# Kernel optimization log

Measured on AMD Instinct MI355X. Metric: run time of the kernel, lower is better.

Reference implementation:

```python
import jax, jax.numpy as jnp
import numpy as np

B, T, DIN, DC, CS = 8, 4096, 1024, 256, 8192
EPS = 1e-12

def _l2norm(x):
    # F.normalize: x / max(||x||_2, eps) along last axis
    n = jnp.sqrt(jnp.sum(x * x, axis=-1, keepdims=True))
    return x / jnp.maximum(n, EPS)

def _wn(v, g):
    # torch weight_norm(dim=0): w = g * v / ||v|| per output row
    n = jnp.sqrt(jnp.sum(v * v, axis=1, keepdims=True))
    return g * v / jnp.maximum(n, EPS)

def setup_inputs() -> dict:
    key = jax.random.key(0)
    k = jax.random.split(key, 4)
    return {
        "z": jax.random.normal(k[0], (B, DIN, T), jnp.float32),
        "in_v": jax.random.normal(k[1], (DC, DIN), jnp.float32) * 0.02,
        "in_g": jnp.ones((DC, 1), jnp.float32),
        "in_b": jnp.zeros((DC,), jnp.float32),
        "out_v": jax.random.normal(k[2], (DIN, DC), jnp.float32) * 0.02,
        "out_g": jnp.ones((DIN, 1), jnp.float32),
        "out_b": jnp.zeros((DIN,), jnp.float32),
        "codebook": jax.random.normal(k[3], (CS, DC), jnp.float32),
    }

def reference(z, in_v, in_g, in_b, out_v, out_g, out_b, codebook):
    b, _, t = z.shape
    w_in = _wn(in_v, in_g)                      # (DC, DIN)
    z_e = jnp.einsum('bdt,cd->bct', z, w_in) + in_b[None, :, None]  # (B, DC, T)

    # decode_latents (eval mode: dropout p=0)
    enc = _l2norm(z_e.transpose(0, 2, 1).reshape(b * t, -1))   # (BT, DC)
    cb = _l2norm(codebook)                                     # (CS, DC)
    dist = (jnp.sum(enc * enc, axis=1, keepdims=True)
            - 2.0 * enc @ cb.T
            + jnp.sum(cb * cb, axis=1)[None, :])               # (BT, CS)
    indices = jnp.argmax(-dist, axis=1).reshape(b, t)          # (B, T)
    z_q = codebook[indices].transpose(0, 2, 1)                 # (B, DC, T)

    commitment_loss = jnp.mean((z_e - jax.lax.stop_gradient(z_q)) ** 2, axis=(1, 2))
    codebook_loss = jnp.mean((z_q - jax.lax.stop_gradient(z_e)) ** 2, axis=(1, 2))

    z_q_st = z_e + jax.lax.stop_gradient(z_q - z_e)            # straight-through
    w_out = _wn(out_v, out_g)                                  # (DIN, DC)
    z_q_out = jnp.einsum('bct,dc->bdt', z_q_st, w_out) + out_b[None, :, None]
    return (z_q_out, commitment_loss, codebook_loss, indices)
```

## Files before the change

kernel.cpp:

```cpp
#include <hip/hip_runtime.h>
#include <stdint.h>

#define BB 8
#define TT 4096
#define DIN 1024
#define DC 256
#define CS 8192
#define EPSF 1e-12f

typedef unsigned short ushort_t;
typedef __attribute__((ext_vector_type(8))) short short8;
typedef __attribute__((ext_vector_type(4))) float f32x4;

constexpr size_t OFF_WIN   = 0;
constexpr size_t OFF_WOUTT = OFF_WIN   + 1048576;
constexpr size_t OFF_CBN   = OFF_WOUTT + 1048576;
constexpr size_t OFF_NRM2  = OFF_CBN   + 8388608;
constexpr size_t OFF_ZE    = OFF_NRM2  + 32768;
constexpr size_t OFF_INV   = OFF_ZE    + 33554432;
constexpr size_t OFF_ENC2  = OFF_INV   + 131072;
constexpr size_t OFF_KEYS  = OFF_ENC2  + 131072;
constexpr size_t OFF_LOSS  = OFF_KEYS  + 262144;
constexpr size_t OFF_WSPL  = OFF_LOSS  + 256;
constexpr size_t OFF_W2T   = OFF_WSPL  + 1048576;
constexpr size_t REQ_WS_ZE = OFF_W2T + 134217728ull;

__device__ __forceinline__ float block_reduce_sum_256(float v, float* sbuf) {
  #pragma unroll
  for (int o = 32; o > 0; o >>= 1) v += __shfl_down(v, o, 64);
  int lane = threadIdx.x & 63, w = threadIdx.x >> 6;
  if (lane == 0) sbuf[w] = v;
  __syncthreads();
  float r = sbuf[0] + sbuf[1] + sbuf[2] + sbuf[3];
  __syncthreads();
  return r;
}

__device__ __forceinline__ ushort_t bf16_rne(float x) {
  unsigned u = __float_as_uint(x);
  unsigned r = (u + 0x7FFFu + ((u >> 16) & 1u)) >> 16;
  return (ushort_t)r;
}
__device__ __forceinline__ float bf16f(ushort_t h) {
  return __uint_as_float(((unsigned)h) << 16);
}

__device__ __forceinline__ int swz4(int r) {
  return (r + (r >> 2)) & 3;
}

__device__ __forceinline__ void async_copy16(const ushort_t* g, ushort_t* lds) {
  __builtin_amdgcn_global_load_lds(
      (const __attribute__((address_space(1))) void*)g,
      (__attribute__((address_space(3))) void*)lds, 16, 0, 0);
}

__device__ __forceinline__ void stage_tile8(const ushort_t* __restrict__ s0,
                                            ushort_t* __restrict__ dstbuf,
                                            const int (&go)[8]) {
  #pragma unroll
  for (int i = 0; i < 8; i++) async_copy16(s0 + go[i], dstbuf + i*512);
}

__device__ __forceinline__ void stage2(const ushort_t* __restrict__ srcbase,
                                       ushort_t* __restrict__ comp,
                                       const int (&go)[2], int wu) {
  async_copy16(srcbase + go[0], comp + wu);
  async_copy16(srcbase + go[1], comp + wu + 4096);
}

#define LD8(base, off) (*(const short8*)((const char*)(base) + (off)))

template<int MH, int CLO>
__device__ __forceinline__ void qmfma(f32x4 (&acc)[8][4],
    const short8 (&fah)[4], const short8 (&fal)[4],
    const short8 (&fbh)[4], const short8 (&fbl)[4]) {
  #pragma unroll
  for (int r = 0; r < 4; r++) {
    #pragma unroll
    for (int c2 = 0; c2 < 2; c2++) {
      f32x4 t = acc[MH*4 + r][CLO + c2];
      t = __builtin_amdgcn_mfma_f32_16x16x32_bf16(fah[r], fbh[CLO + c2], t, 0, 0, 0);
      t = __builtin_amdgcn_mfma_f32_16x16x32_bf16(fal[r], fbh[CLO + c2], t, 0, 0, 0);
      t = __builtin_amdgcn_mfma_f32_16x16x32_bf16(fah[r], fbl[CLO + c2], t, 0, 0, 0);
      acc[MH*4 + r][CLO + c2] = t;
    }
  }
}

__global__ void k_prep_win(const float* __restrict__ v, const float* __restrict__ g,
                           float* __restrict__ w, ushort_t* __restrict__ wh,
                           ushort_t* __restrict__ wl) {
  __shared__ float sb[4];
  int r = blockIdx.x, t = threadIdx.x;
  float xv[4]; float s = 0.f;
  #pragma unroll
  for (int i = 0; i < 4; i++) { xv[i] = v[r*DIN + t + i*256]; s += xv[i]*xv[i]; }
  s = block_reduce_sum_256(s, sb);
  float sc = g[r] / fmaxf(sqrtf(s), EPSF);
  #pragma unroll
  for (int i = 0; i < 4; i++) {
    float val = xv[i] * sc;
    int idx = r*DIN + t + i*256;
    w[idx] = val;
    ushort_t h = bf16_rne(val);
    wh[idx] = h;
    wl[idx] = bf16_rne(val - bf16f(h));
  }
}

__global__ void k_prep_wout(const float* __restrict__ v, const float* __restrict__ g,
                            float* __restrict__ wT) {
  __shared__ float sb[4];
  int r = blockIdx.x, t = threadIdx.x;
  float x = v[r*DC + t];
  float s = block_reduce_sum_256(x*x, sb);
  float sc = g[r] / fmaxf(sqrtf(s), EPSF);
  wT[t*DIN + r] = x * sc;
}

__global__ void k_prep_cb(const float* __restrict__ cb, ushort_t* __restrict__ cbh,
                          ushort_t* __restrict__ cbl, float* __restrict__ nrm2,
                          float* __restrict__ nmraw, float* __restrict__ n2raw,
                          ushort_t* __restrict__ crh, ushort_t* __restrict__ crl) {
  __shared__ float sb[4];
  int j = blockIdx.x, t = threadIdx.x;
  float x = cb[j*DC + t];
  ushort_t hr = bf16_rne(x);
  crh[j*DC + t] = hr;
  crl[j*DC + t] = bf16_rne(x - bf16f(hr));
  float s = block_reduce_sum_256(x*x, sb);
  float nm = fmaxf(sqrtf(s), EPSF);
  float cn = x / nm;
  ushort_t h = bf16_rne(cn);
  cbh[j*DC + t] = h;
  cbl[j*DC + t] = bf16_rne(cn - bf16f(h));
  float q = block_reduce_sum_256(cn*cn, sb);
  if (t == 0) { nrm2[j] = q; nmraw[j] = nm; n2raw[j] = s; }
}

__global__ void k_split_wout(const float* __restrict__ v, const float* __restrict__ g,
                             ushort_t* __restrict__ wh, ushort_t* __restrict__ wl) {
  __shared__ float sb[4];
  int r = blockIdx.x, t = threadIdx.x;
  float x = v[r*DC + t];
  float s = block_reduce_sum_256(x*x, sb);
  float sc = g[r] / fmaxf(sqrtf(s), EPSF);
  float val = x * sc;
  ushort_t h = bf16_rne(val);
  wh[r*DC + t] = h;
  wl[r*DC + t] = bf16_rne(val - bf16f(h));
}

template<bool BIAS>
__global__ __launch_bounds__(256) void k_gemm(
    const float* __restrict__ A, const float* __restrict__ Bmat,
    const float* __restrict__ bias, float* __restrict__ C,
    int K, int lda, int ldb, int ldc, size_t strideB, size_t strideC)
{
  __shared__ float As[16][132];
  __shared__ float Bs[16][132];
  const int bn = blockIdx.x * 128;
  const int bm = blockIdx.y * 128;
  const float* Bb = Bmat + (size_t)blockIdx.z * strideB;
  float* Cb = C + (size_t)blockIdx.z * strideC;
  const int tid = threadIdx.x;
  const int tx = tid & 15, ty = tid >> 4;
  const int am = tid & 127, akq = (tid >> 7) * 8;
  const int bk = tid >> 5, bj = (tid & 31) * 4;

  float acc[8][8];
  #pragma unroll
  for (int i = 0; i < 8; i++)
    #pragma unroll
    for (int j = 0; j < 8; j++) acc[i][j] = 0.f;

  for (int k0 = 0; k0 < K; k0 += 16) {
    float4 a0 = *(const float4*)&A[(size_t)(bm+am)*lda + k0 + akq];
    float4 a1 = *(const float4*)&A[(size_t)(bm+am)*lda + k0 + akq + 4];
    float4 b0 = *(const float4*)&Bb[(size_t)(k0+bk)*ldb + bn + bj];
    float4 b1 = *(const float4*)&Bb[(size_t)(k0+bk+8)*ldb + bn + bj];
    As[akq+0][am] = a0.x; As[akq+1][am] = a0.y; As[akq+2][am] = a0.z; As[akq+3][am] = a0.w;
    As[akq+4][am] = a1.x; As[akq+5][am] = a1.y; As[akq+6][am] = a1.z; As[akq+7][am] = a1.w;
    *(float4*)&Bs[bk][bj] = b0;
    *(float4*)&Bs[bk+8][bj] = b1;
    __syncthreads();
    #pragma unroll
    for (int k = 0; k < 16; k++) {
      float av[8], bv[8];
      float4 x0 = *(const float4*)&As[k][tx*4];
      float4 x1 = *(const float4*)&As[k][tx*4+64];
      float4 y0 = *(const float4*)&Bs[k][ty*4];
      float4 y1 = *(const float4*)&Bs[k][ty*4+64];
      av[0]=x0.x; av[1]=x0.y; av[2]=x0.z; av[3]=x0.w;
      av[4]=x1.x; av[5]=x1.y; av[6]=x1.z; av[7]=x1.w;
      bv[0]=y0.x; bv[1]=y0.y; bv[2]=y0.z; bv[3]=y0.w;
      bv[4]=y1.x; bv[5]=y1.y; bv[6]=y1.z; bv[7]=y1.w;
      #pragma unroll
      for (int i = 0; i < 8; i++)
        #pragma unroll
        for (int j = 0; j < 8; j++)
          acc[i][j] += av[i] * bv[j];
    }
    __syncthreads();
  }

  #pragma unroll
  for (int i = 0; i < 8; i++) {
    int mm = bm + ((i < 4) ? tx*4 + i : 64 + tx*4 + (i-4));
    float bia = BIAS ? bias[mm] : 0.f;
    float4 v0 = make_float4(acc[i][0]+bia, acc[i][1]+bia, acc[i][2]+bia, acc[i][3]+bia);
    float4 v1 = make_float4(acc[i][4]+bia, acc[i][5]+bia, acc[i][6]+bia, acc[i][7]+bia);
    *(float4*)&Cb[(size_t)mm*ldc + bn + ty*4]      = v0;
    *(float4*)&Cb[(size_t)mm*ldc + bn + 64 + ty*4] = v1;
  }
}

__global__ __launch_bounds__(512) void k_ze_enc(
    const float* __restrict__ z,
    const ushort_t* __restrict__ wh, const ushort_t* __restrict__ wl,
    const float* __restrict__ in_b,
    ushort_t* __restrict__ ehi, ushort_t* __restrict__ elo,
    float* __restrict__ inv, float* __restrict__ enc2, float* __restrict__ e2raw)
{
  __shared__ ushort_t smem[49152];
  __shared__ float e2s[128][4];
  __shared__ float sIv[128];

  ushort_t* sAh = smem;
  ushort_t* sAl = smem + 8192;
  ushort_t* sBh = smem + 16384;
  ushort_t* sBl = smem + 32768;

  const int t0 = blockIdx.x * 128;
  const int b  = blockIdx.y;
  const int tid = threadIdx.x;
  const int lane = tid & 63;
  const int wave = tid >> 6;
  const int wr = wave >> 2, wc = wave & 3;
  const int ml = lane & 15, quad = lane >> 4;
  const size_t r0 = (size_t)b*TT + t0;

  const int dl = tid >> 4, tg = tid & 15;
  const float* zsrc = z + (size_t)b*DIN*TT + (size_t)dl*TT + t0 + tg*8;
  int idxA[8];
  #pragma unroll
  for (int i = 0; i < 8; i++) {
    int t = tg*8 + i;
    idxA[i] = t*32 + (((dl >> 3) ^ swz4(t)) << 3) + (dl & 7);
  }

  int goB[2];
  #pragma unroll
  for (int l = 0; l < 2; l++) {
    int chunk = l*512 + tid;
    int r = chunk >> 2, c = chunk & 3;
    int g = c ^ swz4(r);
    goB[l] = r*DIN + (g << 3);
  }
  const int wu = wave * 512;

  int offA[4], offB[4];
  #pragma unroll
  for (int i = 0; i < 4; i++) {
    int r = wr*64 + i*16 + ml;
    int p = quad ^ swz4(r);
    offA[i] = r*64 + p*16;
  }
  #pragma unroll
  for (int i = 0; i < 4; i++) {
    int r = wc*64 + i*16 + ml;
    int p = quad ^ swz4(r);
    offB[i] = r*64 + p*16;
  }

  f32x4 acc[4][4];
  #pragma unroll
  for (int i = 0; i < 4; i++)
    #pragma unroll
    for (int j = 0; j < 4; j++) acc[i][j] = (f32x4)0.f;

  float4 va = *(const float4*)(zsrc);
  float4 vb = *(const float4*)(zsrc + 4);
  stage2(wh, sBh, goB, wu);
  stage2(wl, sBl, goB, wu);
  {
    float vv[8] = {va.x, va.y, va.z, va.w, vb.x, vb.y, vb.z, vb.w};
    #pragma unroll
    for (int i = 0; i < 8; i++) {
      ushort_t h = bf16_rne(vv[i]);
      sAh[idxA[i]] = h;
      sAl[idxA[i]] = bf16_rne(vv[i] - bf16f(h));
    }
  }

  for (int it = 0; it < 32; ++it) {
    __syncthreads();
    const int cbuf = it & 1, nb = cbuf ^ 1;
    if (it < 31) {
      va = *(const float4*)(zsrc + (size_t)(it+1)*32*TT);
      vb = *(const float4*)(zsrc + (size_t)(it+1)*32*TT + 4);
      stage2(wh + (it+1)*32, sBh + nb*8192, goB, wu);
      stage2(wl + (it+1)*32, sBl + nb*8192, goB, wu);
    }
    const char* pAh = (const char*)(sAh + cbuf*4096);
    const char* pAl = (const char*)(sAl + cbuf*4096);
    const char* pBh = (const char*)(sBh + cbuf*8192);
    const char* pBl = (const char*)(sBl + cbuf*8192);

    short8 fbh[4], fbl[4];
    #pragma unroll
    for (int ci = 0; ci < 4; ci++) {
      fbh[ci] = LD8(pBh, offB[ci]);
      fbl[ci] = LD8(pBl, offB[ci]);
    }
    #pragma unroll
    for (int ri = 0; ri < 4; ri++) {
      short8 ah = LD8(pAh, offA[ri]);
      short8 al = LD8(pAl, offA[ri]);
      #pragma unroll
      for (int ci = 0; ci < 4; ci++) {
        acc[ri][ci] = __builtin_amdgcn_mfma_f32_16x16x32_bf16(ah, fbh[ci], acc[ri][ci], 0, 0, 0);
        acc[ri][ci] = __builtin_amdgcn_mfma_f32_16x16x32_bf16(al, fbh[ci], acc[ri][ci], 0, 0, 0);
        acc[ri][ci] = __builtin_amdgcn_mfma_f32_16x16x32_bf16(ah, fbl[ci], acc[ri][ci], 0, 0, 0);
      }
    }

    if (it < 31) {
      ushort_t* dAh = sAh + nb*4096;
      ushort_t* dAl = sAl + nb*4096;
      float vv[8] = {va.x, va.y, va.z, va.w, vb.x, vb.y, vb.z, vb.w};
      #pragma unroll
      for (int i = 0; i < 8; i++) {
        ushort_t h = bf16_rne(vv[i]);
        dAh[idxA[i]] = h;
        dAl[idxA[i]] = bf16_rne(vv[i] - bf16f(h));
      }
    }
  }

  float bia[4];
  #pragma unroll
  for (int ci = 0; ci < 4; ci++) bia[ci] = in_b[wc*64 + ci*16 + ml];

  #pragma unroll
  for (int ri = 0; ri < 4; ri++) {
    #pragma unroll
    for (int reg = 0; reg < 4; reg++) {
      float p = 0.f;
      #pragma unroll
      for (int ci = 0; ci < 4; ci++) {
        float v = acc[ri][ci][reg] + bia[ci];
        acc[ri][ci][reg] = v;
        p += v*v;
      }
      #pragma unroll
      for (int off = 1; off < 16; off <<= 1) p += __shfl_xor(p, off);
      if (ml == 0) e2s[wr*64 + ri*16 + quad*4 + reg][wc] = p;
    }
  }
  __syncthreads();
  if (tid < 128) {
    float s = ((e2s[tid][0] + e2s[tid][1]) + e2s[tid][2]) + e2s[tid][3];
    float iv = 1.f / fmaxf(sqrtf(s), EPSF);
    sIv[tid] = iv;
    inv[r0 + tid]   = iv;
    enc2[r0 + tid]  = (s * iv) * iv;
    e2raw[r0 + tid] = s;
  }
  __syncthreads();

  ushort_t* tb = smem;
  #pragma unroll
  for (int ri = 0; ri < 4; ri++) {
    #pragma unroll
    for (int reg = 0; reg < 4; reg++) {
      int t_loc = wr*64 + ri*16 + quad*4 + reg;
      float ivt = sIv[t_loc];
      #pragma unroll
      for (int ci = 0; ci < 4; ci++) {
        int c_loc = wc*64 + ci*16 + ml;
        tb[t_loc*256 + c_loc] = bf16_rne(acc[ri][ci][reg] * ivt);
      }
    }
  }
  __syncthreads();
  #pragma unroll
  for (int p = 0; p < 8; p++) {
    int ch = p*512 + tid;
    *(short8*)(ehi + r0*DC + (size_t)ch*8) = *(const short8*)(tb + ch*8);
  }
  __syncthreads();
  #pragma unroll
  for (int ri = 0; ri < 4; ri++) {
    #pragma unroll
    for (int reg = 0; reg < 4; reg++) {
      int t_loc = wr*64 + ri*16 + quad*4 + reg;
      float ivt = sIv[t_loc];
      #pragma unroll
      for (int ci = 0; ci < 4; ci++) {
        int c_loc = wc*64 + ci*16 + ml;
        float v = acc[ri][ci][reg] * ivt;
        ushort_t h = bf16_rne(v);
        tb[t_loc*256 + c_loc] = bf16_rne(v - bf16f(h));
      }
    }
  }
  __syncthreads();
  #pragma unroll
  for (int p = 0; p < 8; p++) {
    int ch = p*512 + tid;
    *(short8*)(elo + r0*DC + (size_t)ch*8) = *(const short8*)(tb + ch*8);
  }
}

__global__ __launch_bounds__(256) void k_w2t_mfma(
    const ushort_t* __restrict__ ah_g, const ushort_t* __restrict__ al_g,
    const ushort_t* __restrict__ bh_g, const ushort_t* __restrict__ bl_g,
    float* __restrict__ C)
{
  __shared__ ushort_t As_hi[2][4096];
  __shared__ ushort_t As_lo[2][4096];
  __shared__ ushort_t Bs_hi[2][4096];
  __shared__ ushort_t Bs_lo[2][4096];

  const int m0 = blockIdx.x * 128;
  const int n0 = blockIdx.y * 128;
  const int tid = threadIdx.x;
  const int lane = tid & 63;
  const int wave = tid >> 6;
  const int wr = wave >> 1, wc = wave & 1;
  const int m = lane & 15, quad = lane >> 4;

  const ushort_t* src; ushort_t* dst;
  {
    size_t aoff = (size_t)m0 * DC;
    size_t boff = (size_t)n0 * DC;
    if      (wave == 0) { src = ah_g + aoff; dst = &As_hi[0][0]; }
    else if (wave == 1) { src = al_g + aoff; dst = &As_lo[0][0]; }
    else if (wave == 2) { src = bh_g + boff; dst = &Bs_hi[0][0]; }
    else                { src = bl_g + boff; dst = &Bs_lo[0][0]; }
  }
  const int rr = lane >> 2, cc = lane & 3;

  int goT[8];
  #pragma unroll
  for (int i = 0; i < 8; i++) {
    int r = i*16 + rr;
    int g = cc ^ swz4(r);
    goT[i] = r*DC + (g << 3);
  }

  int offA[4], offB[4];
  #pragma unroll
  for (int ri = 0; ri < 4; ri++) {
    int r = wr*64 + ri*16 + m;
    int p = quad ^ swz4(r);
    offA[ri] = r*64 + p*16;
  }
  #pragma unroll
  for (int ci = 0; ci < 4; ci++) {
    int r = wc*64 + ci*16 + m;
    int p = quad ^ swz4(r);
    offB[ci] = r*64 + p*16;
  }

  f32x4 acc[4][4];
  #pragma unroll
  for (int i = 0; i < 4; i++)
    #pragma unroll
    for (int j = 0; j < 4; j++) acc[i][j] = (f32x4)0.f;

  stage_tile8(src, dst, goT);

  for (int it = 0; it < 8; ++it) {
    __syncthreads();
    if (it < 7) stage_tile8(src + (it+1)*32, dst + ((it+1)&1)*4096, goT);
    const int bo = (it & 1) << 13;

    short8 bh[4], bl[4];
    #pragma unroll
    for (int ci = 0; ci < 4; ci++) {
      bh[ci] = *(const short8*)((const char*)Bs_hi + bo + offB[ci]);
      bl[ci] = *(const short8*)((const char*)Bs_lo + bo + offB[ci]);
    }
    #pragma unroll
    for (int ri = 0; ri < 4; ri++) {
      short8 ah = *(const short8*)((const char*)As_hi + bo + offA[ri]);
      short8 al = *(const short8*)((const char*)As_lo + bo + offA[ri]);
      #pragma unroll
      for (int ci = 0; ci < 4; ci++) {
        acc[ri][ci] = __builtin_amdgcn_mfma_f32_16x16x32_bf16(ah, bh[ci], acc[ri][ci], 0, 0, 0);
        acc[ri][ci] = __builtin_amdgcn_mfma_f32_16x16x32_bf16(al, bh[ci], acc[ri][ci], 0, 0, 0);
        acc[ri][ci] = __builtin_amdgcn_mfma_f32_16x16x32_bf16(ah, bl[ci], acc[ri][ci], 0, 0, 0);
      }
    }
  }

  #pragma unroll
  for (int ri = 0; ri < 4; ri++) {
    int m_loc = wr*64 + ri*16 + quad*4;
    #pragma unroll
    for (int ci = 0; ci < 4; ci++) {
      int n_loc = wc*64 + ci*16 + m;
      #pragma unroll
      for (int reg = 0; reg < 4; reg++) {
        C[(size_t)(m0 + m_loc + reg)*DIN + n0 + n_loc] = acc[ri][ci][reg];
      }
    }
  }
}

__global__ void k_colnorm(const float* __restrict__ ze, float* __restrict__ inv,
                          float* __restrict__ enc2) {
  int r = blockIdx.x * 128 + threadIdx.x;
  int b = r >> 12, t = r & 4095;
  const float* p = ze + (size_t)b*DC*TT + t;
  float s = 0.f;
  for (int c = 0; c < DC; c++) { float x = p[(size_t)c*TT]; s += x*x; }
  float iv = 1.f / fmaxf(sqrtf(s), EPSF);
  inv[r] = iv;
  enc2[r] = (s * iv) * iv;
}

__global__ void k_split_enc(const float* __restrict__ ze, const float* __restrict__ inv,
                            ushort_t* __restrict__ ehi, ushort_t* __restrict__ elo) {
  __shared__ float tile[64][65];
  int b = blockIdx.z, t0 = blockIdx.x * 64, c0 = blockIdx.y * 64;
  int tx = threadIdx.x & 63, ty = threadIdx.x >> 6;
  const float* zb = ze + (size_t)b*DC*TT;
  #pragma unroll
  for (int i = 0; i < 16; i++) {
    int c = i*4 + ty;
    tile[c][tx] = zb[(size_t)(c0+c)*TT + t0 + tx];
  }
  __syncthreads();
  #pragma unroll
  for (int i = 0; i < 16; i++) {
    int t = i*4 + ty;
    float iv = inv[b*TT + t0 + t];
    float val = tile[tx][t] * iv;
    ushort_t h = bf16_rne(val);
    size_t o = ((size_t)(b*TT + t0 + t))*DC + c0 + tx;
    ehi[o] = h;
    elo[o] = bf16_rne(val - bf16f(h));
  }
}

__global__ void k_lossidx(const float* __restrict__ ze, const float* __restrict__ cb,
                          const unsigned long long* __restrict__ keys,
                          float* __restrict__ loss_sums, float* __restrict__ out_idx)
{
  __shared__ float sb[4];
  __shared__ int sj[64];
  int b = blockIdx.y, t0 = blockIdx.x * 64;
  int tid = threadIdx.x;
  if (tid < 64) {
    unsigned long long k = keys[(size_t)b*TT + t0 + tid];
    int j = (int)(unsigned)(k & 0xFFFFFFFFull);
    sj[tid] = j;
    out_idx[(size_t)b*TT + t0 + tid] = (float)j;
  }
  __syncthreads();
  int tt = tid & 63, tc = tid >> 6;
  const float* zb = ze + (size_t)b*DC*TT + t0;
  int j = sj[tt];
  float s = 0.f;
  for (int ci = 0; ci < 64; ci++) {
    int c = tc + ci*4;
    float zev = zb[(size_t)c*TT + tt];
    float zqv = cb[(size_t)j*DC + c];
    float d = zev - zqv;
    s += d*d;
  }
  s = block_reduce_sum_256(s, sb);
  if (tid == 0) atomicAdd(&loss_sums[b], s);
}

__global__ __launch_bounds__(512, 2) void k_dist_mfma(
    const ushort_t* __restrict__ ehi, const ushort_t* __restrict__ elo,
    const ushort_t* __restrict__ cbh, const ushort_t* __restrict__ cbl,
    const float* __restrict__ nrm2, const float* __restrict__ enc2,
    unsigned long long* __restrict__ keys)
{
  __shared__ ushort_t sAh[2][8192];
  __shared__ ushort_t sAl[2][8192];
  __shared__ ushort_t sBh[2][8192];
  __shared__ ushort_t sBl[2][8192];
  __shared__ float sE2[256], sN2[256];
  __shared__ unsigned long long rkey[256];

  const int j0 = blockIdx.x * 256;
  const size_t r0 = (size_t)blockIdx.y * 256;
  const int tid = threadIdx.x;
  const int lane = tid & 63;
  const int wave = tid >> 6;
  const int wr = wave >> 2, wc = wave & 3;
  const int ml = lane & 15, quad = lane >> 4;

  if (tid < 256) {
    sE2[tid] = enc2[r0 + tid];
    sN2[tid] = nrm2[j0 + tid];
    rkey[tid] = 0xFFFFFFFFFFFFFFFFull;
  }

  const ushort_t* gAh = ehi + r0 * DC;
  const ushort_t* gAl = elo + r0 * DC;
  const ushort_t* gBh = cbh + (size_t)j0 * DC;
  const ushort_t* gBl = cbl + (size_t)j0 * DC;

  int goS[2];
  #pragma unroll
  for (int l = 0; l < 2; l++) {
    int chunk = l*512 + tid;
    int r = chunk >> 2, c = chunk & 3;
    int g = c ^ swz4(r);
    goS[l] = r*DC + (g << 3);
  }
  const int wu = wave * 512;

  int offA[8], offB[4];
  #pragma unroll
  for (int i = 0; i < 8; i++) {
    int r = wr*128 + i*16 + ml;
    int p = quad ^ swz4(r);
    offA[i] = r*64 + p*16;
  }
  #pragma unroll
  for (int i = 0; i < 4; i++) {
    int r = wc*64 + i*16 + ml;
    int p = quad ^ swz4(r);
    offB[i] = r*64 + p*16;
  }

  f32x4 acc[8][4];
  #pragma unroll
  for (int i = 0; i < 8; i++)
    #pragma unroll
    for (int j = 0; j < 4; j++) acc[i][j] = (f32x4)0.f;

  stage2(gBh,      &sBh[0][0], goS, wu);
  stage2(gBl,      &sBl[0][0], goS, wu);
  stage2(gAh,      &sAh[0][0], goS, wu);
  stage2(gAl,      &sAl[0][0], goS, wu);
  stage2(gBh + 32, &sBh[1][0], goS, wu);
  stage2(gBl + 32, &sBl[1][0], goS, wu);
  asm volatile("s_waitcnt vmcnt(4)" ::: "memory");
  asm volatile("s_waitcnt lgkmcnt(0)" ::: "memory");
  __builtin_amdgcn_s_barrier();
  __builtin_amdgcn_sched_barrier(0);

  short8 fa_h[4], fa_l[4], fb_h[4], fb_l[4];

  #pragma unroll 2
  for (int k = 0; k < 8; k++) {
    const int cb = k & 1, nb = cb ^ 1;
    const char* pAh = (const char*)&sAh[cb][0];
    const char* pAl = (const char*)&sAl[cb][0];
    const char* pBh = (const char*)&sBh[cb][0];
    const char* pBl = (const char*)&sBl[cb][0];
    __builtin_amdgcn_sched_barrier(0);

    #pragma unroll
    for (int i = 0; i < 4; i++) { fa_h[i] = LD8(pAh, offA[i]); fa_l[i] = LD8(pAl, offA[i]); }
    #pragma unroll
    for (int i = 0; i < 2; i++) { fb_h[i] = LD8(pBh, offB[i]); fb_l[i] = LD8(pBl, offB[i]); }
    if (k < 7) stage2(gAh + (size_t)(k+1)*32, &sAh[nb][0], goS, wu);
    __builtin_amdgcn_s_barrier();
    __builtin_amdgcn_s_setprio(1);
    qmfma<0, 0>(acc, fa_h, fa_l, fb_h, fb_l);
    __builtin_amdgcn_s_setprio(0);
    __builtin_amdgcn_s_barrier();

    #pragma unroll
    for (int i = 2; i < 4; i++) { fb_h[i] = LD8(pBh, offB[i]); fb_l[i] = LD8(pBl, offB[i]); }
    if (k < 7) stage2(gAl + (size_t)(k+1)*32, &sAl[nb][0], goS, wu);
    __builtin_amdgcn_s_barrier();
    __builtin_amdgcn_s_setprio(1);
    qmfma<0, 2>(acc, fa_h, fa_l, fb_h, fb_l);
    __builtin_amdgcn_s_setprio(0);
    __builtin_amdgcn_s_barrier();

    #pragma unroll
    for (int i = 0; i < 4; i++) { fa_h[i] = LD8(pAh, offA[4+i]); fa_l[i] = LD8(pAl, offA[4+i]); }
    if (k < 6) {
      stage2(gBh + (size_t)(k+2)*32, &sBh[cb][0], goS, wu);
      stage2(gBl + (size_t)(k+2)*32, &sBl[cb][0], goS, wu);
    }
    __builtin_amdgcn_s_barrier();
    __builtin_amdgcn_s_setprio(1);
    qmfma<1, 2>(acc, fa_h, fa_l, fb_h, fb_l);
    qmfma<1, 0>(acc, fa_h, fa_l, fb_h, fb_l);
    __builtin_amdgcn_s_setprio(0);
    if (k < 6) { asm volatile("s_waitcnt vmcnt(4)" ::: "memory"); }
    else       { asm volatile("s_waitcnt vmcnt(0)" ::: "memory"); }
    __builtin_amdgcn_s_barrier();
  }

  #pragma unroll
  for (int ri = 0; ri < 8; ri++) {
    #pragma unroll
    for (int reg = 0; reg < 4; reg++) {
      int t_loc = wr*128 + ri*16 + quad*4 + reg;
      float e2 = sE2[t_loc];
      unsigned long long best = 0xFFFFFFFFFFFFFFFFull;
      #pragma unroll
      for (int ci = 0; ci < 4; ci++) {
        int j_loc = wc*64 + ci*16 + ml;
        float d = e2 - 2.0f * acc[ri][ci][reg];
        d = d + sN2[j_loc];
        unsigned long long key =
            ((unsigned long long)__float_as_uint(d) << 32) | (unsigned)(j0 + j_loc);
        best = key < best ? key : best;
      }
      #pragma unroll
      for (int off = 1; off < 16; off <<= 1) {
        unsigned long long o = __shfl_xor(best, off);
        best = o < best ? o : best;
      }
      if (ml == 0) atomicMin(&rkey[t_loc], best);
    }
  }
  __syncthreads();
  if (tid < 256) atomicMin(&keys[r0 + tid], rkey[tid]);
}

__global__ void k_lossrec(const unsigned long long* __restrict__ keys,
                          const float* __restrict__ enc2, const float* __restrict__ nrm2,
                          const float* __restrict__ e2raw, const float* __restrict__ inv,
                          const float* __restrict__ nmraw, const float* __restrict__ n2raw,
                          float* __restrict__ loss_sums, float* __restrict__ out_idx)
{
  __shared__ float sb[4];
  int r = blockIdx.x * 256 + threadIdx.x;
  int b = r >> 12;
  unsigned long long k = keys[r];
  int j = (int)(unsigned)(k & 0xFFFFFFFFull);
  float d = __uint_as_float((unsigned)(k >> 32));
  out_idx[r] = (float)j;
  float dotn = 0.5f * (enc2[r] + nrm2[j] - d);
  float dot_raw = nmraw[j] * dotn / inv[r];
  float le = e2raw[r] - 2.f*dot_raw + n2raw[j];
  float s = block_reduce_sum_256(le, sb);
  if (threadIdx.x == 0) atomicAdd(&loss_sums[b], s);
}

__global__ void k_losswrite(const float* __restrict__ loss_sums, float* __restrict__ out_loss) {
  int i = threadIdx.x;
  if (i < 8) {
    float v = loss_sums[i] * (1.f/1048576.f);
    out_loss[i] = v;
    out_loss[8 + i] = v;
  }
}

__global__ void k_outgather(const float* __restrict__ W2T,
                            const unsigned long long* __restrict__ keys,
                            const float* __restrict__ out_b, float* __restrict__ out)
{
  __shared__ float tile[64][65];
  __shared__ int sj[64];
  int b = blockIdx.y, t0 = blockIdx.x * 64;
  int tid = threadIdx.x;
  if (tid < 64) sj[tid] = (int)(unsigned)(keys[(size_t)b*TT + t0 + tid] & 0xFFFFFFFFull);
  __syncthreads();
  float* ob = out + (size_t)b*DIN*TT;
  int dd = tid & 63, tq = tid >> 6;
  for (int d0 = 0; d0 < DIN; d0 += 64) {
    #pragma unroll
    for (int i = 0; i < 16; i++) {
      int t = tq*16 + i;
      tile[t][dd] = W2T[(size_t)sj[t]*DIN + d0 + dd];
    }
    __syncthreads();
    #pragma unroll
    for (int i = 0; i < 16; i++) {
      int d = tq*16 + i;
      ob[(size_t)(d0+d)*TT + t0 + dd] = tile[dd][d] + out_b[d0+d];
    }
    __syncthreads();
  }
}

extern "C" void kernel_launch(void* const* d_in, const int* in_sizes, int n_in,
                              void* d_out, int out_size, void* d_ws, size_t ws_size,
                              hipStream_t stream) {
  const float* z        = (const float*)d_in[0];
  const float* in_v     = (const float*)d_in[1];
  const float* in_g     = (const float*)d_in[2];
  const float* in_b     = (const float*)d_in[3];
  const float* out_v    = (const float*)d_in[4];
  const float* out_g    = (const float*)d_in[5];
  const float* out_b    = (const float*)d_in[6];
  const float* codebook = (const float*)d_in[7];

  char* w = (char*)d_ws;
  float* w_in   = (float*)(w + OFF_WIN);
  float* w_outT = (float*)(w + OFF_WOUTT);
  float* e2raw  = (float*)(w + OFF_WOUTT);
  float* nmraw  = (float*)(w + OFF_WOUTT + 131072);
  float* n2raw  = (float*)(w + OFF_WOUTT + 163840);
  ushort_t* cb_hi = (ushort_t*)(w + OFF_CBN);
  ushort_t* cb_lo = cb_hi + (size_t)CS*DC;
  float* nrm2   = (float*)(w + OFF_NRM2);
  float* z_e    = (float*)(w + OFF_ZE);
  ushort_t* enc_hi_m = (ushort_t*)(w + OFF_ZE);
  ushort_t* enc_lo_m = enc_hi_m + (size_t)BB*TT*DC;
  float* inv    = (float*)(w + OFF_INV);
  float* enc2   = (float*)(w + OFF_ENC2);
  unsigned long long* keys = (unsigned long long*)(w + OFF_KEYS);
  float* loss_sums = (float*)(w + OFF_LOSS);
  ushort_t* w_hi = (ushort_t*)(w + OFF_WSPL);
  ushort_t* w_lo = w_hi + (size_t)DC*DIN;
  ushort_t* enc_hi_fb = (ushort_t*)(w + OFF_W2T);
  ushort_t* enc_lo_fb = enc_hi_fb + (size_t)BB*TT*DC;
  float* W2T    = (float*)(w + OFF_W2T);
  ushort_t* cbr_hi  = (ushort_t*)(w + OFF_W2T + 33554432);
  ushort_t* cbr_lo  = cbr_hi + (size_t)CS*DC;
  ushort_t* wout_hi = (ushort_t*)(w + OFF_W2T + 33554432 + 8388608);
  ushort_t* wout_lo = wout_hi + (size_t)DIN*DC;

  float* out      = (float*)d_out;
  float* out_loss = out + (size_t)BB*DIN*TT;
  float* out_idx  = out_loss + 16;

  hipMemsetAsync(keys, 0xFF, 32768ull*8, stream);
  hipMemsetAsync(loss_sums, 0, 32, stream);

  const bool mfma_path = (ws_size >= REQ_WS_ZE);

  k_prep_win <<<256, 256, 0, stream>>>(in_v, in_g, w_in, w_hi, w_lo);
  k_prep_cb  <<<8192, 256, 0, stream>>>(codebook, cb_hi, cb_lo, nrm2, nmraw, n2raw,
                                        cbr_hi, cbr_lo);

  if (mfma_path) {
    k_split_wout<<<1024, 256, 0, stream>>>(out_v, out_g, wout_hi, wout_lo);

    k_ze_enc<<<dim3(32, 8), 512, 0, stream>>>(
        z, w_hi, w_lo, in_b, enc_hi_m, enc_lo_m, inv, enc2, e2raw);

    k_dist_mfma<<<dim3(32, 128), 512, 0, stream>>>(
        enc_hi_m, enc_lo_m, cb_hi, cb_lo, nrm2, enc2, keys);

    k_lossrec<<<128, 256, 0, stream>>>(
        keys, enc2, nrm2, e2raw, inv, nmraw, n2raw, loss_sums, out_idx);
    k_losswrite<<<1, 64, 0, stream>>>(loss_sums, out_loss);

    k_w2t_mfma<<<dim3(64, 8), 256, 0, stream>>>(cbr_hi, cbr_lo, wout_hi, wout_lo, W2T);
  } else {
    k_prep_wout<<<1024, 256, 0, stream>>>(out_v, out_g, w_outT);
    k_gemm<true><<<dim3(32, 2, 8), 256, 0, stream>>>(
        w_in, z, in_b, z_e, 1024, 1024, 4096, 4096,
        (size_t)DIN*TT, (size_t)DC*TT);
    k_colnorm<<<256, 128, 0, stream>>>(z_e, inv, enc2);
    k_split_enc<<<dim3(64, 4, 8), 256, 0, stream>>>(z_e, inv, enc_hi_fb, enc_lo_fb);

    k_dist_mfma<<<dim3(32, 128), 512, 0, stream>>>(
        enc_hi_fb, enc_lo_fb, cb_hi, cb_lo, nrm2, enc2, keys);

    k_lossidx<<<dim3(64, 8), 256, 0, stream>>>(z_e, codebook, keys, loss_sums, out_idx);
    k_losswrite<<<1, 64, 0, stream>>>(loss_sums, out_loss);

    k_gemm<false><<<dim3(8, 64, 1), 256, 0, stream>>>(
        codebook, w_outT, nullptr, W2T, 256, 256, 1024, 1024,
        (size_t)0, (size_t)0);
  }

  k_outgather<<<dim3(64, 8), 256, 0, stream>>>(W2T, keys, out_b, out);
}
```

Before: 830.8 us.

## Fuse prep kernels, merge W2T GEMM into distance kernel, fold loss into gather

Merges the w_in, w_out and codebook prep kernels plus the key/loss initialization into one launch, replacing the two memsets. The W2T GEMM now runs as extra blocks of the distance kernel, so both GEMMs share a launch and can fill idle compute units concurrently. Loss and index reconstruction move into the output gather kernel, and the gather now uses float4 loads and stores. This cuts launch count and tail effects, but W2T blocks use only half their 512 threads and grow shared memory use, and loss accumulation now happens through many more atomics.

```diff
diff --git a/kernel.cpp b/kernel.cpp
--- a/kernel.cpp
+++ b/kernel.cpp
@@ -85,6 +85,62 @@
       t = __builtin_amdgcn_mfma_f32_16x16x32_bf16(fah[r], fbl[CLO + c2], t, 0, 0, 0);
       acc[MH*4 + r][CLO + c2] = t;
     }
+  }
+}
+
+__global__ void k_prep_all(
+    const float* __restrict__ in_v, const float* __restrict__ in_g,
+    float* __restrict__ w_in, ushort_t* __restrict__ wh, ushort_t* __restrict__ wl,
+    const float* __restrict__ out_v, const float* __restrict__ out_g,
+    ushort_t* __restrict__ wouth, ushort_t* __restrict__ woutl,
+    const float* __restrict__ cb, ushort_t* __restrict__ cbh, ushort_t* __restrict__ cbl,
+    float* __restrict__ nrm2, float* __restrict__ nmraw, float* __restrict__ n2raw,
+    ushort_t* __restrict__ crh, ushort_t* __restrict__ crl,
+    unsigned long long* __restrict__ keys, float* __restrict__ loss_sums)
+{
+  __shared__ float sb[4];
+  const int bx = blockIdx.x, t = threadIdx.x;
+  if (bx < 256) {
+    if (bx == 0 && t < 8) loss_sums[t] = 0.f;
+    int r = bx;
+    float xv[4]; float s = 0.f;
+    #pragma unroll
+    for (int i = 0; i < 4; i++) { xv[i] = in_v[r*DIN + t + i*256]; s += xv[i]*xv[i]; }
+    s = block_reduce_sum_256(s, sb);
+    float sc = in_g[r] / fmaxf(sqrtf(s), EPSF);
+    #pragma unroll
+    for (int i = 0; i < 4; i++) {
+      float val = xv[i] * sc;
+      int idx = r*DIN + t + i*256;
+      w_in[idx] = val;
+      ushort_t h = bf16_rne(val);
+      wh[idx] = h;
+      wl[idx] = bf16_rne(val - bf16f(h));
+    }
+  } else if (bx < 1280) {
+    int r = bx - 256;
+    float x = out_v[r*DC + t];
+    float s = block_reduce_sum_256(x*x, sb);
+    float sc = out_g[r] / fmaxf(sqrtf(s), EPSF);
+    float val = x * sc;
+    ushort_t h = bf16_rne(val);
+    wouth[r*DC + t] = h;
+    woutl[r*DC + t] = bf16_rne(val - bf16f(h));
+  } else {
+    int j = bx - 1280;
+    if (t < 4) keys[(size_t)j*4 + t] = 0xFFFFFFFFFFFFFFFFull;
+    float x = cb[j*DC + t];
+    ushort_t hr = bf16_rne(x);
+    crh[j*DC + t] = hr;
+    crl[j*DC + t] = bf16_rne(x - bf16f(hr));
+    float s = block_reduce_sum_256(x*x, sb);
+    float nm = fmaxf(sqrtf(s), EPSF);
+    float cn = x / nm;
+    ushort_t h = bf16_rne(cn);
+    cbh[j*DC + t] = h;
+    cbl[j*DC + t] = bf16_rne(cn - bf16f(h));
+    float q = block_reduce_sum_256(cn*cn, sb);
+    if (t == 0) { nrm2[j] = q; nmraw[j] = nm; n2raw[j] = s; }
   }
 }
 
@@ -139,19 +195,6 @@
   if (t == 0) { nrm2[j] = q; nmraw[j] = nm; n2raw[j] = s; }
 }
 
-__global__ void k_split_wout(const float* __restrict__ v, const float* __restrict__ g,
-                             ushort_t* __restrict__ wh, ushort_t* __restrict__ wl) {
-  __shared__ float sb[4];
-  int r = blockIdx.x, t = threadIdx.x;
-  float x = v[r*DC + t];
-  float s = block_reduce_sum_256(x*x, sb);
-  float sc = g[r] / fmaxf(sqrtf(s), EPSF);
-  float val = x * sc;
-  ushort_t h = bf16_rne(val);
-  wh[r*DC + t] = h;
-  wl[r*DC + t] = bf16_rne(val - bf16f(h));
-}
-
 template<bool BIAS>
 __global__ __launch_bounds__(256) void k_gemm(
     const float* __restrict__ A, const float* __restrict__ Bmat,
@@ -414,98 +457,243 @@
   }
 }
 
-__global__ __launch_bounds__(256) void k_w2t_mfma(
-    const ushort_t* __restrict__ ah_g, const ushort_t* __restrict__ al_g,
-    const ushort_t* __restrict__ bh_g, const ushort_t* __restrict__ bl_g,
-    float* __restrict__ C)
+__global__ __launch_bounds__(512, 2) void k_dist_mfma(
+    const ushort_t* __restrict__ ehi, const ushort_t* __restrict__ elo,
+    const ushort_t* __restrict__ cbh, const ushort_t* __restrict__ cbl,
+    const float* __restrict__ nrm2, const float* __restrict__ enc2,
+    unsigned long long* __restrict__ keys,
+    const ushort_t* __restrict__ crh, const ushort_t* __restrict__ crl,
+    const ushort_t* __restrict__ wouth, const ushort_t* __restrict__ woutl,
+    float* __restrict__ W2T)
 {
-  __shared__ ushort_t As_hi[2][4096];
-  __shared__ ushort_t As_lo[2][4096];
-  __shared__ ushort_t Bs_hi[2][4096];
-  __shared__ ushort_t Bs_lo[2][4096];
-
-  const int m0 = blockIdx.x * 128;
-  const int n0 = blockIdx.y * 128;
+  __shared__ ushort_t sAh[2][8192];
+  __shared__ ushort_t sAl[2][8192];
+  __shared__ ushort_t sBh[2][8192];
+  __shared__ ushort_t sBl[2][8192];
+  __shared__ float sE2[256], sN2[256];
+  __shared__ unsigned long long rkey[256];
+
   const int tid = threadIdx.x;
   const int lane = tid & 63;
   const int wave = tid >> 6;
-  const int wr = wave >> 1, wc = wave & 1;
-  const int m = lane & 15, quad = lane >> 4;
-
-  const ushort_t* src; ushort_t* dst;
-  {
-    size_t aoff = (size_t)m0 * DC;
-    size_t boff = (size_t)n0 * DC;
-    if      (wave == 0) { src = ah_g + aoff; dst = &As_hi[0][0]; }
-    else if (wave == 1) { src = al_g + aoff; dst = &As_lo[0][0]; }
-    else if (wave == 2) { src = bh_g + boff; dst = &Bs_hi[0][0]; }
-    else                { src = bl_g + boff; dst = &Bs_lo[0][0]; }
-  }
-  const int rr = lane >> 2, cc = lane & 3;
-
-  int goT[8];
-  #pragma unroll
-  for (int i = 0; i < 8; i++) {
-    int r = i*16 + rr;
-    int g = cc ^ swz4(r);
-    goT[i] = r*DC + (g << 3);
-  }
-
-  int offA[4], offB[4];
-  #pragma unroll
-  for (int ri = 0; ri < 4; ri++) {
-    int r = wr*64 + ri*16 + m;
-    int p = quad ^ swz4(r);
-    offA[ri] = r*64 + p*16;
-  }
-  #pragma unroll
-  for (int ci = 0; ci < 4; ci++) {
-    int r = wc*64 + ci*16 + m;
-    int p = quad ^ swz4(r);
-    offB[ci] = r*64 + p*16;
-  }
-
-  f32x4 acc[4][4];
-  #pragma unroll
-  for (int i = 0; i < 4; i++)
-    #pragma unroll
-    for (int j = 0; j < 4; j++) acc[i][j] = (f32x4)0.f;
-
-  stage_tile8(src, dst, goT);
-
-  for (int it = 0; it < 8; ++it) {
+  const int ml = lane & 15, quad = lane >> 4;
+
+  if (blockIdx.x < 4096) {
+    const int bid = blockIdx.x;
+    const int j0 = (bid & 31) * 256;
+    const size_t r0 = (size_t)(bid >> 5) * 256;
+    const int wr = wave >> 2, wc = wave & 3;
+
+    if (tid < 256) {
+      sE2[tid] = enc2[r0 + tid];
+      sN2[tid] = nrm2[j0 + tid];
+      rkey[tid] = 0xFFFFFFFFFFFFFFFFull;
+    }
+
+    const ushort_t* gAh = ehi + r0 * DC;
+    const ushort_t* gAl = elo + r0 * DC;
+    const ushort_t* gBh = cbh + (size_t)j0 * DC;
+    const ushort_t* gBl = cbl + (size_t)j0 * DC;
+
+    int goS[2];
+    #pragma unroll
+    for (int l = 0; l < 2; l++) {
+      int chunk = l*512 + tid;
+      int r = chunk >> 2, c = chunk & 3;
+      int g = c ^ swz4(r);
+      goS[l] = r*DC + (g << 3);
+    }
+    const int wu = wave * 512;
+
+    int offA[8], offB[4];
+    #pragma unroll
+    for (int i = 0; i < 8; i++) {
+      int r = wr*128 + i*16 + ml;
+      int p = quad ^ swz4(r);
+      offA[i] = r*64 + p*16;
+    }
+    #pragma unroll
+    for (int i = 0; i < 4; i++) {
+      int r = wc*64 + i*16 + ml;
+      int p = quad ^ swz4(r);
+      offB[i] = r*64 + p*16;
+    }
+
+    f32x4 acc[8][4];
+    #pragma unroll
+    for (int i = 0; i < 8; i++)
+      #pragma unroll
+      for (int j = 0; j < 4; j++) acc[i][j] = (f32x4)0.f;
+
+    stage2(gBh,      &sBh[0][0], goS, wu);
+    stage2(gBl,      &sBl[0][0], goS, wu);
+    stage2(gAh,      &sAh[0][0], goS, wu);
+    stage2(gAl,      &sAl[0][0], goS, wu);
+    stage2(gBh + 32, &sBh[1][0], goS, wu);
+    stage2(gBl + 32, &sBl[1][0], goS, wu);
+    asm volatile("s_waitcnt vmcnt(4)" ::: "memory");
+    asm volatile("s_waitcnt lgkmcnt(0)" ::: "memory");
+    __builtin_amdgcn_s_barrier();
+    __builtin_amdgcn_sched_barrier(0);
+
+    short8 fa_h[4], fa_l[4], fb_h[4], fb_l[4];
+
+    #pragma unroll 2
+    for (int k = 0; k < 8; k++) {
+      const int cb = k & 1, nb = cb ^ 1;
+      const char* pAh = (const char*)&sAh[cb][0];
+      const char* pAl = (const char*)&sAl[cb][0];
+      const char* pBh = (const char*)&sBh[cb][0];
+      const char* pBl = (const char*)&sBl[cb][0];
+      __builtin_amdgcn_sched_barrier(0);
+
+      #pragma unroll
+      for (int i = 0; i < 4; i++) { fa_h[i] = LD8(pAh, offA[i]); fa_l[i] = LD8(pAl, offA[i]); }
+      #pragma unroll
+      for (int i = 0; i < 2; i++) { fb_h[i] = LD8(pBh, offB[i]); fb_l[i] = LD8(pBl, offB[i]); }
+      if (k < 7) stage2(gAh + (size_t)(k+1)*32, &sAh[nb][0], goS, wu);
+      __builtin_amdgcn_s_barrier();
+      __builtin_amdgcn_s_setprio(1);
+      qmfma<0, 0>(acc, fa_h, fa_l, fb_h, fb_l);
+      __builtin_amdgcn_s_setprio(0);
+      __builtin_amdgcn_s_barrier();
+
+      #pragma unroll
+      for (int i = 2; i < 4; i++) { fb_h[i] = LD8(pBh, offB[i]); fb_l[i] = LD8(pBl, offB[i]); }
+      if (k < 7) stage2(gAl + (size_t)(k+1)*32, &sAl[nb][0], goS, wu);
+      __builtin_amdgcn_s_barrier();
+      __builtin_amdgcn_s_setprio(1);
+      qmfma<0, 2>(acc, fa_h, fa_l, fb_h, fb_l);
+      __builtin_amdgcn_s_setprio(0);
+      __builtin_amdgcn_s_barrier();
+
+      #pragma unroll
+      for (int i = 0; i < 4; i++) { fa_h[i] = LD8(pAh, offA[4+i]); fa_l[i] = LD8(pAl, offA[4+i]); }
+      if (k < 6) {
+        stage2(gBh + (size_t)(k+2)*32, &sBh[cb][0], goS, wu);
+        stage2(gBl + (size_t)(k+2)*32, &sBl[cb][0], goS, wu);
+      }
+      __builtin_amdgcn_s_barrier();
+      __builtin_amdgcn_s_setprio(1);
+      qmfma<1, 2>(acc, fa_h, fa_l, fb_h, fb_l);
+      qmfma<1, 0>(acc, fa_h, fa_l, fb_h, fb_l);
+      __builtin_amdgcn_s_setprio(0);
+      if (k < 6) { asm volatile("s_waitcnt vmcnt(4)" ::: "memory"); }
+      else       { asm volatile("s_waitcnt vmcnt(0)" ::: "memory"); }
+      __builtin_amdgcn_s_barrier();
+    }
+
+    #pragma unroll
+    for (int ri = 0; ri < 8; ri++) {
+      #pragma unroll
+      for (int reg = 0; reg < 4; reg++) {
+        int t_loc = wr*128 + ri*16 + quad*4 + reg;
+        float e2 = sE2[t_loc];
+        unsigned long long best = 0xFFFFFFFFFFFFFFFFull;
+        #pragma unroll
+        for (int ci = 0; ci < 4; ci++) {
+          int j_loc = wc*64 + ci*16 + ml;
+          float d = e2 - 2.0f * acc[ri][ci][reg];
+          d = d + sN2[j_loc];
+          unsigned long long key =
+              ((unsigned long long)__float_as_uint(d) << 32) | (unsigned)(j0 + j_loc);
+          best = key < best ? key : best;
+        }
+        #pragma unroll
+        for (int off = 1; off < 16; off <<= 1) {
+          unsigned long long o = __shfl_xor(best, off);
+          best = o < best ? o : best;
+        }
+        if (ml == 0) atomicMin(&rkey[t_loc], best);
+      }
+    }
     __syncthreads();
-    if (it < 7) stage_tile8(src + (it+1)*32, dst + ((it+1)&1)*4096, goT);
-    const int bo = (it & 1) << 13;
-
-    short8 bh[4], bl[4];
+    if (tid < 256) atomicMin(&keys[r0 + tid], rkey[tid]);
+  } else {
+    const int id = blockIdx.x - 4096;
+    const int m0 = (id & 63) * 128;
+    const int n0 = (id >> 6) * 128;
+    const bool act = tid < 256;
+    const int wr = (wave & 3) >> 1, wc = wave & 1;
+    const int rr = lane >> 2, cc = lane & 3;
+
+    const ushort_t* src = crh; ushort_t* dst = &sAh[0][0];
+    {
+      size_t aoff = (size_t)m0 * DC;
+      size_t boff = (size_t)n0 * DC;
+      if      (wave == 0) { src = crh + aoff;   dst = &sAh[0][0]; }
+      else if (wave == 1) { src = crl + aoff;   dst = &sAl[0][0]; }
+      else if (wave == 2) { src = wouth + boff; dst = &sBh[0][0]; }
+      else if (wave == 3) { src = woutl + boff; dst = &sBl[0][0]; }
+    }
+
+    int goT[8];
+    #pragma unroll
+    for (int i = 0; i < 8; i++) {
+      int r = i*16 + rr;
+      int g = cc ^ swz4(r);
+      goT[i] = r*DC + (g << 3);
+    }
+
+    int offA[4], offB[4];
+    #pragma unroll
+    for (int ri = 0; ri < 4; ri++) {
+      int r = wr*64 + ri*16 + ml;
+      int p = quad ^ swz4(r);
+      offA[ri] = r*64 + p*16;
+    }
     #pragma unroll
     for (int ci = 0; ci < 4; ci++) {
-      bh[ci] = *(const short8*)((const char*)Bs_hi + bo + offB[ci]);
-      bl[ci] = *(const short8*)((const char*)Bs_lo + bo + offB[ci]);
-    }
-    #pragma unroll
-    for (int ri = 0; ri < 4; ri++) {
-      short8 ah = *(const short8*)((const char*)As_hi + bo + offA[ri]);
-      short8 al = *(const short8*)((const char*)As_lo + bo + offA[ri]);
-      #pragma unroll
-      for (int ci = 0; ci < 4; ci++) {
-        acc[ri][ci] = __builtin_amdgcn_mfma_f32_16x16x32_bf16(ah, bh[ci], acc[ri][ci], 0, 0, 0);
-        acc[ri][ci] = __builtin_amdgcn_mfma_f32_16x16x32_bf16(al, bh[ci], acc[ri][ci], 0, 0, 0);
-        acc[ri][ci] = __builtin_amdgcn_mfma_f32_16x16x32_bf16(ah, bl[ci], acc[ri][ci], 0, 0, 0);
+      int r = wc*64 + ci*16 + ml;
+      int p = quad ^ swz4(r);
+      offB[ci] = r*64 + p*16;
+    }
+
+    f32x4 acc[4][4];
+    #pragma unroll
+    for (int i = 0; i < 4; i++)
+      #pragma unroll
+      for (int j = 0; j < 4; j++) acc[i][j] = (f32x4)0.f;
+
+    if (act) stage_tile8(src, dst, goT);
+
+    for (int it = 0; it < 8; ++it) {
+      __syncthreads();
+      if (act && it < 7) stage_tile8(src + (it+1)*32, dst + ((it+1)&1)*4096, goT);
+      const int bo = (it & 1) << 13;
+      if (act) {
+        short8 bh[4], bl[4];
+        #pragma unroll
+        for (int ci = 0; ci < 4; ci++) {
+          bh[ci] = *(const short8*)((const char*)&sBh[0][0] + bo + offB[ci]);
+          bl[ci] = *(const short8*)((const char*)&sBl[0][0] + bo + offB[ci]);
+        }
+        #pragma unroll
+        for (int ri = 0; ri < 4; ri++) {
+          short8 ah = *(const short8*)((const char*)&sAh[0][0] + bo + offA[ri]);
+          short8 al = *(const short8*)((const char*)&sAl[0][0] + bo + offA[ri]);
+          #pragma unroll
+          for (int ci = 0; ci < 4; ci++) {
+            acc[ri][ci] = __builtin_amdgcn_mfma_f32_16x16x32_bf16(ah, bh[ci], acc[ri][ci], 0, 0, 0);
+            acc[ri][ci] = __builtin_amdgcn_mfma_f32_16x16x32_bf16(al, bh[ci], acc[ri][ci], 0, 0, 0);
+            acc[ri][ci] = __builtin_amdgcn_mfma_f32_16x16x32_bf16(ah, bl[ci], acc[ri][ci], 0, 0, 0);
+          }
+        }
       }
     }
-  }
-
-  #pragma unroll
-  for (int ri = 0; ri < 4; ri++) {
-    int m_loc = wr*64 + ri*16 + quad*4;
-    #pragma unroll
-    for (int ci = 0; ci < 4; ci++) {
-      int n_loc = wc*64 + ci*16 + m;
-      #pragma unroll
-      for (int reg = 0; reg < 4; reg++) {
-        C[(size_t)(m0 + m_loc + reg)*DIN + n0 + n_loc] = acc[ri][ci][reg];
+
+    if (act) {
+      #pragma unroll
+      for (int ri = 0; ri < 4; ri++) {
+        int m_loc = wr*64 + ri*16 + quad*4;
+        #pragma unroll
+        for (int ci = 0; ci < 4; ci++) {
+          int n_loc = wc*64 + ci*16 + ml;
+          #pragma unroll
+          for (int reg = 0; reg < 4; reg++) {
+            W2T[(size_t)(m0 + m_loc + reg)*DIN + n0 + n_loc] = acc[ri][ci][reg];
+          }
+        }
       }
     }
   }
@@ -577,7 +765,7 @@
   if (tid == 0) atomicAdd(&loss_sums[b], s);
 }
 
-__global__ __launch_bounds__(512, 2) void k_dist_mfma(
+__global__ __launch_bounds__(512, 2) void k_dist_fb(
     const ushort_t* __restrict__ ehi, const ushort_t* __restrict__ elo,
     const ushort_t* __restrict__ cbh, const ushort_t* __restrict__ cbl,
     const float* __restrict__ nrm2, const float* __restrict__ enc2,
@@ -725,26 +913,6 @@
   if (tid < 256) atomicMin(&keys[r0 + tid], rkey[tid]);
 }
 
-__global__ void k_lossrec(const unsigned long long* __restrict__ keys,
-                          const float* __restrict__ enc2, const float* __restrict__ nrm2,
-                          const float* __restrict__ e2raw, const float* __restrict__ inv,
-                          const float* __restrict__ nmraw, const float* __restrict__ n2raw,
-                          float* __restrict__ loss_sums, float* __restrict__ out_idx)
-{
-  __shared__ float sb[4];
-  int r = blockIdx.x * 256 + threadIdx.x;
-  int b = r >> 12;
-  unsigned long long k = keys[r];
-  int j = (int)(unsigned)(k & 0xFFFFFFFFull);
-  float d = __uint_as_float((unsigned)(k >> 32));
-  out_idx[r] = (float)j;
-  float dotn = 0.5f * (enc2[r] + nrm2[j] - d);
-  float dot_raw = nmraw[j] * dotn / inv[r];
-  float le = e2raw[r] - 2.f*dot_raw + n2raw[j];
-  float s = block_reduce_sum_256(le, sb);
-  if (threadIdx.x == 0) atomicAdd(&loss_sums[b], s);
-}
-
 __global__ void k_losswrite(const float* __restrict__ loss_sums, float* __restrict__ out_loss) {
   int i = threadIdx.x;
   if (i < 8) {
@@ -754,29 +922,57 @@
   }
 }
 
+template<bool WITH_LOSS>
 __global__ void k_outgather(const float* __restrict__ W2T,
                             const unsigned long long* __restrict__ keys,
-                            const float* __restrict__ out_b, float* __restrict__ out)
+                            const float* __restrict__ out_b, float* __restrict__ out,
+                            const float* __restrict__ enc2, const float* __restrict__ nrm2,
+                            const float* __restrict__ e2raw, const float* __restrict__ inv,
+                            const float* __restrict__ nmraw, const float* __restrict__ n2raw,
+                            float* __restrict__ loss_sums, float* __restrict__ out_idx)
 {
   __shared__ float tile[64][65];
   __shared__ int sj[64];
   int b = blockIdx.y, t0 = blockIdx.x * 64;
   int tid = threadIdx.x;
-  if (tid < 64) sj[tid] = (int)(unsigned)(keys[(size_t)b*TT + t0 + tid] & 0xFFFFFFFFull);
+  if (tid < 64) {
+    size_t r = (size_t)b*TT + t0 + tid;
+    unsigned long long k = keys[r];
+    int j = (int)(unsigned)(k & 0xFFFFFFFFull);
+    sj[tid] = j;
+    if (WITH_LOSS) {
+      out_idx[r] = (float)j;
+      float d = __uint_as_float((unsigned)(k >> 32));
+      float dotn = 0.5f * (enc2[r] + nrm2[j] - d);
+      float dot_raw = nmraw[j] * dotn / inv[r];
+      float le = e2raw[r] - 2.f*dot_raw + n2raw[j];
+      #pragma unroll
+      for (int o = 32; o > 0; o >>= 1) le += __shfl_down(le, o, 64);
+      if (tid == 0) atomicAdd(&loss_sums[b], le);
+    }
+  }
   __syncthreads();
   float* ob = out + (size_t)b*DIN*TT;
-  int dd = tid & 63, tq = tid >> 6;
+  const int tg = tid >> 4;
+  const int d4 = (tid & 15) * 4;
+  const int t4 = tid & 15;
+  const int dq = tid >> 4;
   for (int d0 = 0; d0 < DIN; d0 += 64) {
     #pragma unroll
-    for (int i = 0; i < 16; i++) {
-      int t = tq*16 + i;
-      tile[t][dd] = W2T[(size_t)sj[t]*DIN + d0 + dd];
+    for (int i = 0; i < 4; i++) {
+      int t = i*16 + tg;
+      float4 v = *(const float4*)&W2T[(size_t)sj[t]*DIN + d0 + d4];
+      tile[t][d4+0] = v.x; tile[t][d4+1] = v.y;
+      tile[t][d4+2] = v.z; tile[t][d4+3] = v.w;
     }
     __syncthreads();
     #pragma unroll
-    for (int i = 0; i < 16; i++) {
-      int d = tq*16 + i;
-      ob[(size_t)(d0+d)*TT + t0 + dd] = tile[dd][d] + out_b[d0+d];
+    for (int i = 0; i < 4; i++) {
+      int d = i*16 + dq;
+      float bia = out_b[d0+d];
+      float4 v = make_float4(tile[t4*4+0][d]+bia, tile[t4*4+1][d]+bia,
+                             tile[t4*4+2][d]+bia, tile[t4*4+3][d]+bia);
+      *(float4*)&ob[(size_t)(d0+d)*TT + t0 + t4*4] = v;
     }
     __syncthreads();
   }
@@ -824,30 +1020,34 @@
   float* out_loss = out + (size_t)BB*DIN*TT;
   float* out_idx  = out_loss + 16;
 
-  hipMemsetAsync(keys, 0xFF, 32768ull*8, stream);
-  hipMemsetAsync(loss_sums, 0, 32, stream);
-
   const bool mfma_path = (ws_size >= REQ_WS_ZE);
 
-  k_prep_win <<<256, 256, 0, stream>>>(in_v, in_g, w_in, w_hi, w_lo);
-  k_prep_cb  <<<8192, 256, 0, stream>>>(codebook, cb_hi, cb_lo, nrm2, nmraw, n2raw,
-                                        cbr_hi, cbr_lo);
-
   if (mfma_path) {
-    k_split_wout<<<1024, 256, 0, stream>>>(out_v, out_g, wout_hi, wout_lo);
+    k_prep_all<<<9472, 256, 0, stream>>>(
+        in_v, in_g, w_in, w_hi, w_lo,
+        out_v, out_g, wout_hi, wout_lo,
+        codebook, cb_hi, cb_lo, nrm2, nmraw, n2raw, cbr_hi, cbr_lo,
+        keys, loss_sums);
 
     k_ze_enc<<<dim3(32, 8), 512, 0, stream>>>(
         z, w_hi, w_lo, in_b, enc_hi_m, enc_lo_m, inv, enc2, e2raw);
 
-    k_dist_mfma<<<dim3(32, 128), 512, 0, stream>>>(
-        enc_hi_m, enc_lo_m, cb_hi, cb_lo, nrm2, enc2, keys);
-
-    k_lossrec<<<128, 256, 0, stream>>>(
-        keys, enc2, nrm2, e2raw, inv, nmraw, n2raw, loss_sums, out_idx);
+    k_dist_mfma<<<4608, 512, 0, stream>>>(
+        enc_hi_m, enc_lo_m, cb_hi, cb_lo, nrm2, enc2, keys,
+        cbr_hi, cbr_lo, wout_hi, wout_lo, W2T);
+
+    k_outgather<true><<<dim3(64, 8), 256, 0, stream>>>(
+        W2T, keys, out_b, out,
+        enc2, nrm2, e2raw, inv, nmraw, n2raw, loss_sums, out_idx);
+
     k_losswrite<<<1, 64, 0, stream>>>(loss_sums, out_loss);
-
-    k_w2t_mfma<<<dim3(64, 8), 256, 0, stream>>>(cbr_hi, cbr_lo, wout_hi, wout_lo, W2T);
   } else {
+    hipMemsetAsync(keys, 0xFF, 32768ull*8, stream);
+    hipMemsetAsync(loss_sums, 0, 32, stream);
+
+    k_prep_win <<<256, 256, 0, stream>>>(in_v, in_g, w_in, w_hi, w_lo);
+    k_prep_cb  <<<8192, 256, 0, stream>>>(codebook, cb_hi, cb_lo, nrm2, nmraw, n2raw,
+                                          cbr_hi, cbr_lo);
     k_prep_wout<<<1024, 256, 0, stream>>>(out_v, out_g, w_outT);
     k_gemm<true><<<dim3(32, 2, 8), 256, 0, stream>>>(
         w_in, z, in_b, z_e, 1024, 1024, 4096, 4096,
@@ -855,7 +1055,7 @@
     k_colnorm<<<256, 128, 0, stream>>>(z_e, inv, enc2);
     k_split_enc<<<dim3(64, 4, 8), 256, 0, stream>>>(z_e, inv, enc_hi_fb, enc_lo_fb);
 
-    k_dist_mfma<<<dim3(32, 128), 512, 0, stream>>>(
+    k_dist_fb<<<dim3(32, 128), 512, 0, stream>>>(
         enc_hi_fb, enc_lo_fb, cb_hi, cb_lo, nrm2, enc2, keys);
 
     k_lossidx<<<dim3(64, 8), 256, 0, stream>>>(z_e, codebook, keys, loss_sums, out_idx);
@@ -864,7 +1064,9 @@
     k_gemm<false><<<dim3(8, 64, 1), 256, 0, stream>>>(
         codebook, w_outT, nullptr, W2T, 256, 256, 1024, 1024,
         (size_t)0, (size_t)0);
-  }
-
-  k_outgather<<<dim3(64, 8), 256, 0, stream>>>(W2T, keys, out_b, out);
-}
+
+    k_outgather<false><<<dim3(64, 8), 256, 0, stream>>>(
+        W2T, keys, out_b, out,
+        nullptr, nullptr, nullptr, nullptr, nullptr, nullptr, nullptr, nullptr);
+  }
+}
```

New measurement: 766.8 us. -7.7%, faster.
